# Kernel tuning notes

Hardware: AMD Instinct MI355X
Metric: run time of the kernel (lower is better)

The kernel has to match this reference:

```python
import jax, jax.numpy as jnp
import numpy as np

NOISE_STD = 0.05
ALPHA = 0.2

B, T, I, H, O, R = 64, 1024, 8, 512, 2, 2


def setup_inputs() -> dict:
    key = jax.random.key(0)
    ks = jax.random.split(key, 6)
    return {
        "input": jax.random.normal(ks[0], (B, T, I), dtype=jnp.float32),
        "noise": jax.random.normal(ks[1], (B, T, H), dtype=jnp.float32),
        "wi": jax.random.normal(ks[2], (I, H), dtype=jnp.float32),
        "si": jnp.ones((I,), dtype=jnp.float32),
        "m": jax.random.normal(ks[3], (H, R), dtype=jnp.float32),
        "n": jax.random.normal(ks[4], (H, R), dtype=jnp.float32),
        "wo": jax.random.normal(ks[5], (H, O), dtype=jnp.float32) * 4.0,
        "so": jnp.ones((O,), dtype=jnp.float32),
        "h0": jnp.zeros((H,), dtype=jnp.float32),
    }


def reference(input, noise, wi, si, m, n, wo, so, h0):
    batch, seq_len, _ = input.shape
    hidden = m.shape[0]
    wi_full = wi * si[:, None]          # (I, H)
    wo_full = wo * so                   # (H, O)
    # Precompute input projection for all timesteps: (B, T, H)
    inp_proj = jnp.einsum('bti,ih->bth', input, wi_full)
    h_init = jnp.broadcast_to(h0, (batch, hidden))
    r_init = jnp.tanh(h_init)

    def step(carry, xs):
        h, r = carry
        nz, p = xs  # (B, H) each
        rec = (r @ n) @ m.T / hidden    # rank-r recurrent drive
        h = h + NOISE_STD * nz + ALPHA * (-h + rec + p)
        r = jnp.tanh(h)
        out = r @ wo_full / hidden      # (B, O)
        return (h, r), (out, h)

    xs = (jnp.swapaxes(noise, 0, 1), jnp.swapaxes(inp_proj, 0, 1))  # time-major
    _, (output, traj) = jax.lax.scan(step, (h_init, r_init), xs)
    return jnp.swapaxes(output, 0, 1), jnp.swapaxes(traj, 0, 1)
```

## Files before the change

kernel.cpp:

```cpp
#include <hip/hip_runtime.h>
#include <cstddef>

constexpr int B = 64, T = 1024, I = 8, H = 512, O = 2;
constexpr float ALPHA = 0.2f;
constexpr float NOISE_STD = 0.05f;

constexpr int PF = 8;

template <int CTRL>
__device__ __forceinline__ float dpp_add(float x) {
    int y = __builtin_amdgcn_update_dpp(0, __float_as_int(x), CTRL, 0xF, 0xF, true);
    return x + __int_as_float(y);
}

__device__ __forceinline__ float wave_sum_to_lane63(float x) {
    x = dpp_add<0x111>(x);
    x = dpp_add<0x112>(x);
    x = dpp_add<0x114>(x);
    x = dpp_add<0x118>(x);
    x = dpp_add<0x142>(x);
    x = dpp_add<0x143>(x);
    return x;
}

__device__ __forceinline__ float bcast63(float x) {
    return __int_as_float(__builtin_amdgcn_readlane(__float_as_int(x), 63));
}

__device__ __forceinline__ float fast_tanh(float x) {
    float z = __builtin_amdgcn_exp2f(x * 2.885390081777927f);
    return fmaf(-2.0f, __builtin_amdgcn_rcpf(z + 1.0f), 1.0f);
}

__global__ __launch_bounds__(128)
void precompute_d_kernel(const float* __restrict__ input,
                         const float* __restrict__ noise,
                         const float* __restrict__ wi,
                         const float* __restrict__ si,
                         float* __restrict__ d) {
    const int    bt = blockIdx.x;
    const int    hq = threadIdx.x << 2;

    float x[I];
#pragma unroll
    for (int i = 0; i < I; ++i) x[i] = input[(size_t)bt * I + i] * si[i];

    const size_t off = (size_t)bt * H + hq;
    const float4 nz  = *(const float4*)(noise + off);

    float4 p = make_float4(0.f, 0.f, 0.f, 0.f);
#pragma unroll
    for (int i = 0; i < I; ++i) {
        const float4 w = *(const float4*)(wi + i * H + hq);
        p.x = fmaf(x[i], w.x, p.x);
        p.y = fmaf(x[i], w.y, p.y);
        p.z = fmaf(x[i], w.z, p.z);
        p.w = fmaf(x[i], w.w, p.w);
    }
    float4 o;
    o.x = fmaf(NOISE_STD, nz.x, ALPHA * p.x);
    o.y = fmaf(NOISE_STD, nz.y, ALPHA * p.y);
    o.z = fmaf(NOISE_STD, nz.z, ALPHA * p.z);
    o.w = fmaf(NOISE_STD, nz.w, ALPHA * p.w);
    *(float4*)(d + off) = o;
}

template <bool FUSED>
__global__ __launch_bounds__(64)
void rnn_kernel(const float* __restrict__ dbuf,
                const float* __restrict__ input,
                const float* __restrict__ wi,
                const float* __restrict__ si,
                const float* __restrict__ m,
                const float* __restrict__ n,
                const float* __restrict__ wo,
                const float* __restrict__ so,
                const float* __restrict__ h0,
                float* __restrict__ out,
                float* __restrict__ traj)
{
    const int b    = blockIdx.x;
    const int lane = threadIdx.x;

    constexpr float RS  = ALPHA / (float)H;
    constexpr float OMA = 1.0f - ALPHA;

    const float so0 = so[0] / (float)H;
    const float so1 = so[1] / (float)H;

    float m0s[8], m1s[8], n0[8], n1[8], wo0s[8], wo1s[8], h[8], r[8];
    float wif[I][8];

#pragma unroll
    for (int k = 0; k < 2; ++k) {
#pragma unroll
        for (int c = 0; c < 4; ++c) {
            const int s = k * 4 + c;
            const int j = 256 * k + 4 * lane + c;
            m0s[s]  = m[2 * j + 0] * RS;
            m1s[s]  = m[2 * j + 1] * RS;
            n0[s]   = n[2 * j + 0];
            n1[s]   = n[2 * j + 1];
            wo0s[s] = wo[2 * j + 0] * so0;
            wo1s[s] = wo[2 * j + 1] * so1;
            h[s]    = h0[j];
            r[s]    = tanhf(h[s]);
            if (FUSED) {
#pragma unroll
                for (int i = 0; i < I; ++i) wif[i][s] = wi[i * H + j] * si[i];
            }
        }
    }

    const float* pd    = dbuf + (size_t)b * T * H + 4 * lane;
    float*       ptraj = traj + (size_t)b * T * H + 4 * lane;
    const float* pin   = input + (size_t)b * T * I;
    float*       pout  = out + (size_t)b * T * O;

    float4 buf0[PF], buf1[PF];
#pragma unroll
    for (int u = 0; u < PF; ++u) {
        buf0[u] = *(const float4*)(pd + (size_t)u * H);
        buf1[u] = *(const float4*)(pd + (size_t)u * H + 256);
    }

    static_assert(T % PF == 0, "T must be a multiple of PF");

    for (int tb = 0; tb < T; tb += PF) {
#pragma unroll
        for (int u = 0; u < PF; ++u) {
            const int t = tb + u;

            const float4 cur0 = buf0[u];
            const float4 cur1 = buf1[u];
            if (t + PF < T) {
                buf0[u] = *(const float4*)(pd + (size_t)(t + PF) * H);
                buf1[u] = *(const float4*)(pd + (size_t)(t + PF) * H + 256);
            }

            float pa0a = 0.f, pa1a = 0.f, po0a = 0.f, po1a = 0.f;
            float pa0b = 0.f, pa1b = 0.f, po0b = 0.f, po1b = 0.f;
#pragma unroll
            for (int s = 0; s < 4; ++s) {
                pa0a = fmaf(r[s], n0[s], pa0a);
                pa1a = fmaf(r[s], n1[s], pa1a);
                po0a = fmaf(r[s], wo0s[s], po0a);
                po1a = fmaf(r[s], wo1s[s], po1a);
                pa0b = fmaf(r[s + 4], n0[s + 4], pa0b);
                pa1b = fmaf(r[s + 4], n1[s + 4], pa1b);
                po0b = fmaf(r[s + 4], wo0s[s + 4], po0b);
                po1b = fmaf(r[s + 4], wo1s[s + 4], po1b);
            }
            float ra0 = wave_sum_to_lane63(pa0a + pa0b);
            float ra1 = wave_sum_to_lane63(pa1a + pa1b);
            float ro0 = wave_sum_to_lane63(po0a + po0b);
            float ro1 = wave_sum_to_lane63(po1a + po1b);

            float dv[8];
            if (!FUSED) {
                dv[0] = cur0.x; dv[1] = cur0.y; dv[2] = cur0.z; dv[3] = cur0.w;
                dv[4] = cur1.x; dv[5] = cur1.y; dv[6] = cur1.z; dv[7] = cur1.w;
            } else {
                float x[I];
#pragma unroll
                for (int i = 0; i < I; ++i) x[i] = pin[(size_t)t * I + i];
                const float nzv[8] = {cur0.x, cur0.y, cur0.z, cur0.w,
                                      cur1.x, cur1.y, cur1.z, cur1.w};
#pragma unroll
                for (int s = 0; s < 8; ++s) {
                    float p = 0.f;
#pragma unroll
                    for (int i = 0; i < I; ++i) p = fmaf(x[i], wif[i][s], p);
                    dv[s] = fmaf(NOISE_STD, nzv[s], ALPHA * p);
                }
            }
            float pre[8];
#pragma unroll
            for (int s = 0; s < 8; ++s) pre[s] = fmaf(h[s], OMA, dv[s]);

            if (lane == 63 && t > 0) {
                *(float2*)(pout + (size_t)(t - 1) * O) = make_float2(ro0, ro1);
            }

            const float a0 = bcast63(ra0);
            const float a1 = bcast63(ra1);

#pragma unroll
            for (int s = 0; s < 8; ++s) {
                h[s] = fmaf(a1, m1s[s], fmaf(a0, m0s[s], pre[s]));
                r[s] = fast_tanh(h[s]);
            }

            *(float4*)(ptraj + (size_t)t * H + 0)   = make_float4(h[0], h[1], h[2], h[3]);
            *(float4*)(ptraj + (size_t)t * H + 256) = make_float4(h[4], h[5], h[6], h[7]);
        }
    }

    float po0 = 0.f, po1 = 0.f;
#pragma unroll
    for (int s = 0; s < 8; ++s) {
        po0 = fmaf(r[s], wo0s[s], po0);
        po1 = fmaf(r[s], wo1s[s], po1);
    }
    po0 = wave_sum_to_lane63(po0);
    po1 = wave_sum_to_lane63(po1);
    if (lane == 63) {
        *(float2*)(pout + (size_t)(T - 1) * O) = make_float2(po0, po1);
    }
}

extern "C" void kernel_launch(void* const* d_in, const int* in_sizes, int n_in,
                              void* d_out, int out_size, void* d_ws, size_t ws_size,
                              hipStream_t stream) {
    const float* input = (const float*)d_in[0];
    const float* noise = (const float*)d_in[1];
    const float* wi    = (const float*)d_in[2];
    const float* si    = (const float*)d_in[3];
    const float* m     = (const float*)d_in[4];
    const float* n     = (const float*)d_in[5];
    const float* wo    = (const float*)d_in[6];
    const float* so    = (const float*)d_in[7];
    const float* h0    = (const float*)d_in[8];

    float* out  = (float*)d_out;
    float* traj = (float*)d_out + (size_t)B * T * O;

    const size_t d_bytes = (size_t)B * T * H * sizeof(float);

    if (ws_size >= d_bytes) {
        float* dbuf = (float*)d_ws;
        precompute_d_kernel<<<B * T, 128, 0, stream>>>(input, noise, wi, si, dbuf);
        rnn_kernel<false><<<B, 64, 0, stream>>>(dbuf, nullptr, nullptr, nullptr,
                                                m, n, wo, so, h0, out, traj);
    } else {
        rnn_kernel<true><<<B, 64, 0, stream>>>(noise, input, wi, si,
                                               m, n, wo, so, h0, out, traj);
    }
}
```

Measured before the change: 608.2 us.

## Split recurrence across four waves per batch and move output projection to separate kernel

The sequential recurrence kernel now uses 256 threads (four waves) per batch row, so each lane owns 2 hidden units instead of 8. The rank-2 partial sums are combined through double-buffered shared memory with one __syncthreads per step. The output projection (tanh of traj times wo) is removed from the serial loop and computed afterwards by a fully parallel kernel that rereads traj. This shortens the per-step critical path, at the cost of a block barrier each step and an extra pass over the trajectory. The fallback fused kernel is also restructured into a simple one-step prefetch loop.

```diff
diff --git a/kernel.cpp b/kernel.cpp
--- a/kernel.cpp
+++ b/kernel.cpp
@@ -65,19 +65,125 @@
     *(float4*)(d + off) = o;
 }
 
-template <bool FUSED>
-__global__ __launch_bounds__(64)
-void rnn_kernel(const float* __restrict__ dbuf,
-                const float* __restrict__ input,
-                const float* __restrict__ wi,
-                const float* __restrict__ si,
-                const float* __restrict__ m,
-                const float* __restrict__ n,
+__global__ __launch_bounds__(256)
+void rnn4_kernel(const float* __restrict__ dbuf,
+                 const float* __restrict__ m,
+                 const float* __restrict__ n,
+                 const float* __restrict__ h0,
+                 float* __restrict__ traj)
+{
+    const int b    = blockIdx.x;
+    const int w    = threadIdx.x >> 6;
+    const int lane = threadIdx.x & 63;
+    const int j0   = w * 128 + 2 * lane;
+
+    constexpr float RS  = ALPHA / (float)H;
+    constexpr float OMA = 1.0f - ALPHA;
+
+    const float4 mv = *(const float4*)(m + 2 * j0);
+    const float4 nv = *(const float4*)(n + 2 * j0);
+    const float mm0[2] = {mv.x * RS, mv.z * RS};
+    const float mm1[2] = {mv.y * RS, mv.w * RS};
+    const float nn0[2] = {nv.x, nv.z};
+    const float nn1[2] = {nv.y, nv.w};
+
+    const float2 h0v = *(const float2*)(h0 + j0);
+    float h[2] = {h0v.x, h0v.y};
+    float r[2] = {tanhf(h[0]), tanhf(h[1])};
+
+    __shared__ float2 part[2][4];
+
+    const float* pd = dbuf + (size_t)b * T * H + j0;
+    float*       pt = traj + (size_t)b * T * H + j0;
+
+    float2 ring[PF];
+#pragma unroll
+    for (int u = 0; u < PF; ++u) ring[u] = *(const float2*)(pd + (size_t)u * H);
+
+    static_assert(T % PF == 0, "T must be a multiple of PF");
+
+    for (int tb = 0; tb < T; tb += PF) {
+#pragma unroll
+        for (int u = 0; u < PF; ++u) {
+            const int t = tb + u;
+
+            const float2 d = ring[u];
+            if (t + PF < T) ring[u] = *(const float2*)(pd + (size_t)(t + PF) * H);
+
+            float pa0 = fmaf(r[1], nn0[1], r[0] * nn0[0]);
+            float pa1 = fmaf(r[1], nn1[1], r[0] * nn1[0]);
+            pa0 = wave_sum_to_lane63(pa0);
+            pa1 = wave_sum_to_lane63(pa1);
+            if (lane == 63) part[t & 1][w] = make_float2(pa0, pa1);
+
+            const float pre0 = fmaf(h[0], OMA, d.x);
+            const float pre1 = fmaf(h[1], OMA, d.y);
+
+            __syncthreads();
+
+            const float4 q0 = *(const float4*)&part[t & 1][0];
+            const float4 q1 = *(const float4*)&part[t & 1][2];
+            const float a0 = (q0.x + q0.z) + (q1.x + q1.z);
+            const float a1 = (q0.y + q0.w) + (q1.y + q1.w);
+
+            h[0] = fmaf(a1, mm1[0], fmaf(a0, mm0[0], pre0));
+            h[1] = fmaf(a1, mm1[1], fmaf(a0, mm0[1], pre1));
+            r[0] = fast_tanh(h[0]);
+            r[1] = fast_tanh(h[1]);
+
+            *(float2*)(pt + (size_t)t * H) = make_float2(h[0], h[1]);
+        }
+    }
+}
+
+__global__ __launch_bounds__(256)
+void out_kernel(const float* __restrict__ traj,
                 const float* __restrict__ wo,
                 const float* __restrict__ so,
-                const float* __restrict__ h0,
-                float* __restrict__ out,
-                float* __restrict__ traj)
+                float* __restrict__ out) {
+    const int bt   = blockIdx.x * 4 + (threadIdx.x >> 6);
+    const int lane = threadIdx.x & 63;
+
+    const float so0 = so[0] / (float)H;
+    const float so1 = so[1] / (float)H;
+
+    const float* pt = traj + (size_t)bt * H;
+
+    float o0 = 0.f, o1 = 0.f;
+#pragma unroll
+    for (int k = 0; k < 2; ++k) {
+        const int j = 256 * k + 4 * lane;
+        const float4 hv = *(const float4*)(pt + j);
+        const float4 w0 = *(const float4*)(wo + 2 * j);
+        const float4 w1 = *(const float4*)(wo + 2 * j + 4);
+        const float r0 = fast_tanh(hv.x);
+        const float r1 = fast_tanh(hv.y);
+        const float r2 = fast_tanh(hv.z);
+        const float r3 = fast_tanh(hv.w);
+        o0 = fmaf(r0, w0.x, o0); o1 = fmaf(r0, w0.y, o1);
+        o0 = fmaf(r1, w0.z, o0); o1 = fmaf(r1, w0.w, o1);
+        o0 = fmaf(r2, w1.x, o0); o1 = fmaf(r2, w1.y, o1);
+        o0 = fmaf(r3, w1.z, o0); o1 = fmaf(r3, w1.w, o1);
+    }
+    o0 = wave_sum_to_lane63(o0);
+    o1 = wave_sum_to_lane63(o1);
+    if (lane == 63) {
+        *(float2*)(out + (size_t)bt * O) = make_float2(o0 * so0, o1 * so1);
+    }
+}
+
+__global__ __launch_bounds__(64)
+void rnn_fused_kernel(const float* __restrict__ noise,
+                      const float* __restrict__ input,
+                      const float* __restrict__ wi,
+                      const float* __restrict__ si,
+                      const float* __restrict__ m,
+                      const float* __restrict__ n,
+                      const float* __restrict__ wo,
+                      const float* __restrict__ so,
+                      const float* __restrict__ h0,
+                      float* __restrict__ out,
+                      float* __restrict__ traj)
 {
     const int b    = blockIdx.x;
     const int lane = threadIdx.x;
@@ -105,95 +211,78 @@
             wo1s[s] = wo[2 * j + 1] * so1;
             h[s]    = h0[j];
             r[s]    = tanhf(h[s]);
-            if (FUSED) {
-#pragma unroll
-                for (int i = 0; i < I; ++i) wif[i][s] = wi[i * H + j] * si[i];
-            }
-        }
-    }
-
-    const float* pd    = dbuf + (size_t)b * T * H + 4 * lane;
+#pragma unroll
+            for (int i = 0; i < I; ++i) wif[i][s] = wi[i * H + j] * si[i];
+        }
+    }
+
+    const float* pn    = noise + (size_t)b * T * H + 4 * lane;
     float*       ptraj = traj + (size_t)b * T * H + 4 * lane;
     const float* pin   = input + (size_t)b * T * I;
     float*       pout  = out + (size_t)b * T * O;
 
-    float4 buf0[PF], buf1[PF];
-#pragma unroll
-    for (int u = 0; u < PF; ++u) {
-        buf0[u] = *(const float4*)(pd + (size_t)u * H);
-        buf1[u] = *(const float4*)(pd + (size_t)u * H + 256);
-    }
-
-    static_assert(T % PF == 0, "T must be a multiple of PF");
-
-    for (int tb = 0; tb < T; tb += PF) {
-#pragma unroll
-        for (int u = 0; u < PF; ++u) {
-            const int t = tb + u;
-
-            const float4 cur0 = buf0[u];
-            const float4 cur1 = buf1[u];
-            if (t + PF < T) {
-                buf0[u] = *(const float4*)(pd + (size_t)(t + PF) * H);
-                buf1[u] = *(const float4*)(pd + (size_t)(t + PF) * H + 256);
-            }
-
-            float pa0a = 0.f, pa1a = 0.f, po0a = 0.f, po1a = 0.f;
-            float pa0b = 0.f, pa1b = 0.f, po0b = 0.f, po1b = 0.f;
-#pragma unroll
-            for (int s = 0; s < 4; ++s) {
-                pa0a = fmaf(r[s], n0[s], pa0a);
-                pa1a = fmaf(r[s], n1[s], pa1a);
-                po0a = fmaf(r[s], wo0s[s], po0a);
-                po1a = fmaf(r[s], wo1s[s], po1a);
-                pa0b = fmaf(r[s + 4], n0[s + 4], pa0b);
-                pa1b = fmaf(r[s + 4], n1[s + 4], pa1b);
-                po0b = fmaf(r[s + 4], wo0s[s + 4], po0b);
-                po1b = fmaf(r[s + 4], wo1s[s + 4], po1b);
-            }
-            float ra0 = wave_sum_to_lane63(pa0a + pa0b);
-            float ra1 = wave_sum_to_lane63(pa1a + pa1b);
-            float ro0 = wave_sum_to_lane63(po0a + po0b);
-            float ro1 = wave_sum_to_lane63(po1a + po1b);
-
-            float dv[8];
-            if (!FUSED) {
-                dv[0] = cur0.x; dv[1] = cur0.y; dv[2] = cur0.z; dv[3] = cur0.w;
-                dv[4] = cur1.x; dv[5] = cur1.y; dv[6] = cur1.z; dv[7] = cur1.w;
-            } else {
-                float x[I];
-#pragma unroll
-                for (int i = 0; i < I; ++i) x[i] = pin[(size_t)t * I + i];
-                const float nzv[8] = {cur0.x, cur0.y, cur0.z, cur0.w,
-                                      cur1.x, cur1.y, cur1.z, cur1.w};
-#pragma unroll
-                for (int s = 0; s < 8; ++s) {
-                    float p = 0.f;
-#pragma unroll
-                    for (int i = 0; i < I; ++i) p = fmaf(x[i], wif[i][s], p);
-                    dv[s] = fmaf(NOISE_STD, nzv[s], ALPHA * p);
-                }
-            }
-            float pre[8];
-#pragma unroll
-            for (int s = 0; s < 8; ++s) pre[s] = fmaf(h[s], OMA, dv[s]);
-
-            if (lane == 63 && t > 0) {
-                *(float2*)(pout + (size_t)(t - 1) * O) = make_float2(ro0, ro1);
-            }
-
-            const float a0 = bcast63(ra0);
-            const float a1 = bcast63(ra1);
-
-#pragma unroll
-            for (int s = 0; s < 8; ++s) {
-                h[s] = fmaf(a1, m1s[s], fmaf(a0, m0s[s], pre[s]));
-                r[s] = fast_tanh(h[s]);
-            }
-
-            *(float4*)(ptraj + (size_t)t * H + 0)   = make_float4(h[0], h[1], h[2], h[3]);
-            *(float4*)(ptraj + (size_t)t * H + 256) = make_float4(h[4], h[5], h[6], h[7]);
-        }
+    float4 cur0 = *(const float4*)(pn + 0);
+    float4 cur1 = *(const float4*)(pn + 256);
+
+    for (int t = 0; t < T; ++t) {
+        float4 nxt0, nxt1;
+        if (t + 1 < T) {
+            nxt0 = *(const float4*)(pn + (size_t)(t + 1) * H);
+            nxt1 = *(const float4*)(pn + (size_t)(t + 1) * H + 256);
+        }
+
+        float pa0a = 0.f, pa1a = 0.f, po0a = 0.f, po1a = 0.f;
+        float pa0b = 0.f, pa1b = 0.f, po0b = 0.f, po1b = 0.f;
+#pragma unroll
+        for (int s = 0; s < 4; ++s) {
+            pa0a = fmaf(r[s], n0[s], pa0a);
+            pa1a = fmaf(r[s], n1[s], pa1a);
+            po0a = fmaf(r[s], wo0s[s], po0a);
+            po1a = fmaf(r[s], wo1s[s], po1a);
+            pa0b = fmaf(r[s + 4], n0[s + 4], pa0b);
+            pa1b = fmaf(r[s + 4], n1[s + 4], pa1b);
+            po0b = fmaf(r[s + 4], wo0s[s + 4], po0b);
+            po1b = fmaf(r[s + 4], wo1s[s + 4], po1b);
+        }
+        float ra0 = wave_sum_to_lane63(pa0a + pa0b);
+        float ra1 = wave_sum_to_lane63(pa1a + pa1b);
+        float ro0 = wave_sum_to_lane63(po0a + po0b);
+        float ro1 = wave_sum_to_lane63(po1a + po1b);
+
+        if (lane == 63 && t > 0) {
+            *(float2*)(pout + (size_t)(t - 1) * O) = make_float2(ro0, ro1);
+        }
+
+        const float a0 = bcast63(ra0);
+        const float a1 = bcast63(ra1);
+
+        float x[I];
+#pragma unroll
+        for (int i = 0; i < I; ++i) x[i] = pin[(size_t)t * I + i];
+        const float nzv[8] = {cur0.x, cur0.y, cur0.z, cur0.w,
+                              cur1.x, cur1.y, cur1.z, cur1.w};
+        float dv[8];
+#pragma unroll
+        for (int s = 0; s < 8; ++s) {
+            float p = 0.f;
+#pragma unroll
+            for (int i = 0; i < I; ++i) p = fmaf(x[i], wif[i][s], p);
+            dv[s] = fmaf(NOISE_STD, nzv[s], ALPHA * p);
+        }
+
+#pragma unroll
+        for (int s = 0; s < 8; ++s) {
+            float tmp = fmaf(a0, m0s[s], dv[s]);
+            tmp       = fmaf(a1, m1s[s], tmp);
+            h[s]      = fmaf(h[s], OMA, tmp);
+            r[s]      = fast_tanh(h[s]);
+        }
+
+        *(float4*)(ptraj + (size_t)t * H + 0)   = make_float4(h[0], h[1], h[2], h[3]);
+        *(float4*)(ptraj + (size_t)t * H + 256) = make_float4(h[4], h[5], h[6], h[7]);
+
+        cur0 = nxt0;
+        cur1 = nxt1;
     }
 
     float po0 = 0.f, po1 = 0.f;
@@ -230,10 +319,10 @@
     if (ws_size >= d_bytes) {
         float* dbuf = (float*)d_ws;
         precompute_d_kernel<<<B * T, 128, 0, stream>>>(input, noise, wi, si, dbuf);
-        rnn_kernel<false><<<B, 64, 0, stream>>>(dbuf, nullptr, nullptr, nullptr,
-                                                m, n, wo, so, h0, out, traj);
+        rnn4_kernel<<<B, 256, 0, stream>>>(dbuf, m, n, h0, traj);
+        out_kernel<<<(B * T) / 4, 256, 0, stream>>>(traj, wo, so, out);
     } else {
-        rnn_kernel<true><<<B, 64, 0, stream>>>(noise, input, wi, si,
+        rnn_fused_kernel<<<B, 64, 0, stream>>>(noise, input, wi, si,
                                                m, n, wo, so, h0, out, traj);
     }
 }
```

After: 587.3 us. 3.4% less time.

## Fuse input projection into RNN and split hidden state across four waves per batch

Applied to the files above, without the earlier changes.

Removes the separate precompute kernel and its round trip through a large workspace buffer. The scan kernel now runs 256 threads per batch row, with each lane owning two hidden units, and computes the input projection on the fly from inputs staged in LDS. Each timestep reduces across the four waves through a double-buffered LDS array guarded by a workgroup barrier. This shortens the serial dependency chain and the per-lane work, at the cost of one block barrier per timestep.

```diff
diff --git a/kernel.cpp b/kernel.cpp
--- a/kernel.cpp
+++ b/kernel.cpp
@@ -23,106 +23,74 @@
     return x;
 }
 
-__device__ __forceinline__ float bcast63(float x) {
-    return __int_as_float(__builtin_amdgcn_readlane(__float_as_int(x), 63));
-}
-
 __device__ __forceinline__ float fast_tanh(float x) {
     float z = __builtin_amdgcn_exp2f(x * 2.885390081777927f);
     return fmaf(-2.0f, __builtin_amdgcn_rcpf(z + 1.0f), 1.0f);
 }
 
-__global__ __launch_bounds__(128)
-void precompute_d_kernel(const float* __restrict__ input,
-                         const float* __restrict__ noise,
-                         const float* __restrict__ wi,
-                         const float* __restrict__ si,
-                         float* __restrict__ d) {
-    const int    bt = blockIdx.x;
-    const int    hq = threadIdx.x << 2;
-
-    float x[I];
-#pragma unroll
-    for (int i = 0; i < I; ++i) x[i] = input[(size_t)bt * I + i] * si[i];
-
-    const size_t off = (size_t)bt * H + hq;
-    const float4 nz  = *(const float4*)(noise + off);
-
-    float4 p = make_float4(0.f, 0.f, 0.f, 0.f);
-#pragma unroll
-    for (int i = 0; i < I; ++i) {
-        const float4 w = *(const float4*)(wi + i * H + hq);
-        p.x = fmaf(x[i], w.x, p.x);
-        p.y = fmaf(x[i], w.y, p.y);
-        p.z = fmaf(x[i], w.z, p.z);
-        p.w = fmaf(x[i], w.w, p.w);
-    }
-    float4 o;
-    o.x = fmaf(NOISE_STD, nz.x, ALPHA * p.x);
-    o.y = fmaf(NOISE_STD, nz.y, ALPHA * p.y);
-    o.z = fmaf(NOISE_STD, nz.z, ALPHA * p.z);
-    o.w = fmaf(NOISE_STD, nz.w, ALPHA * p.w);
-    *(float4*)(d + off) = o;
-}
-
-template <bool FUSED>
-__global__ __launch_bounds__(64)
-void rnn_kernel(const float* __restrict__ dbuf,
-                const float* __restrict__ input,
-                const float* __restrict__ wi,
-                const float* __restrict__ si,
-                const float* __restrict__ m,
-                const float* __restrict__ n,
-                const float* __restrict__ wo,
-                const float* __restrict__ so,
-                const float* __restrict__ h0,
-                float* __restrict__ out,
-                float* __restrict__ traj)
+__global__ __launch_bounds__(256)
+void rnn_fused4_kernel(const float* __restrict__ input,
+                       const float* __restrict__ noise,
+                       const float* __restrict__ wi,
+                       const float* __restrict__ si,
+                       const float* __restrict__ m,
+                       const float* __restrict__ n,
+                       const float* __restrict__ wo,
+                       const float* __restrict__ so,
+                       const float* __restrict__ h0,
+                       float* __restrict__ out,
+                       float* __restrict__ traj)
 {
     const int b    = blockIdx.x;
-    const int lane = threadIdx.x;
+    const int w    = threadIdx.x >> 6;
+    const int lane = threadIdx.x & 63;
+    const int j0   = w * 128 + 2 * lane;
+
+    __shared__ float  xin[T * I];
+    __shared__ float4 part[2][4];
+
+    {
+        const float4* src = (const float4*)(input + (size_t)b * T * I);
+        float4*       dst = (float4*)xin;
+#pragma unroll
+        for (int i = 0; i < (T * I / 4) / 256; ++i)
+            dst[threadIdx.x + 256 * i] = src[threadIdx.x + 256 * i];
+    }
+    __syncthreads();
 
     constexpr float RS  = ALPHA / (float)H;
     constexpr float OMA = 1.0f - ALPHA;
-
     const float so0 = so[0] / (float)H;
     const float so1 = so[1] / (float)H;
 
-    float m0s[8], m1s[8], n0[8], n1[8], wo0s[8], wo1s[8], h[8], r[8];
-    float wif[I][8];
-
-#pragma unroll
-    for (int k = 0; k < 2; ++k) {
-#pragma unroll
-        for (int c = 0; c < 4; ++c) {
-            const int s = k * 4 + c;
-            const int j = 256 * k + 4 * lane + c;
-            m0s[s]  = m[2 * j + 0] * RS;
-            m1s[s]  = m[2 * j + 1] * RS;
-            n0[s]   = n[2 * j + 0];
-            n1[s]   = n[2 * j + 1];
-            wo0s[s] = wo[2 * j + 0] * so0;
-            wo1s[s] = wo[2 * j + 1] * so1;
-            h[s]    = h0[j];
-            r[s]    = tanhf(h[s]);
-            if (FUSED) {
-#pragma unroll
-                for (int i = 0; i < I; ++i) wif[i][s] = wi[i * H + j] * si[i];
-            }
-        }
-    }
-
-    const float* pd    = dbuf + (size_t)b * T * H + 4 * lane;
-    float*       ptraj = traj + (size_t)b * T * H + 4 * lane;
-    const float* pin   = input + (size_t)b * T * I;
-    float*       pout  = out + (size_t)b * T * O;
-
-    float4 buf0[PF], buf1[PF];
-#pragma unroll
-    for (int u = 0; u < PF; ++u) {
-        buf0[u] = *(const float4*)(pd + (size_t)u * H);
-        buf1[u] = *(const float4*)(pd + (size_t)u * H + 256);
-    }
+    const float4 mv = *(const float4*)(m + 2 * j0);
+    const float4 nv = *(const float4*)(n + 2 * j0);
+    const float4 wv = *(const float4*)(wo + 2 * j0);
+    const float mm0[2] = {mv.x * RS, mv.z * RS};
+    const float mm1[2] = {mv.y * RS, mv.w * RS};
+    const float nn0[2] = {nv.x, nv.z};
+    const float nn1[2] = {nv.y, nv.w};
+    const float ww0[2] = {wv.x, wv.z};
+    const float ww1[2] = {wv.y, wv.w};
+
+    float wif[I][2];
+#pragma unroll
+    for (int i = 0; i < I; ++i) {
+        wif[i][0] = wi[i * H + j0]     * si[i];
+        wif[i][1] = wi[i * H + j0 + 1] * si[i];
+    }
+
+    const float2 h0v = *(const float2*)(h0 + j0);
+    float h[2] = {h0v.x, h0v.y};
+    float r[2] = {tanhf(h[0]), tanhf(h[1])};
+
+    const float* pn   = noise + (size_t)b * T * H + j0;
+    float*       pt   = traj  + (size_t)b * T * H + j0;
+    float*       pout = out   + (size_t)b * T * O;
+
+    float2 ring[PF];
+#pragma unroll
+    for (int u = 0; u < PF; ++u) ring[u] = *(const float2*)(pn + (size_t)u * H);
 
     static_assert(T % PF == 0, "T must be a multiple of PF");
 
@@ -131,81 +99,84 @@
         for (int u = 0; u < PF; ++u) {
             const int t = tb + u;
 
-            const float4 cur0 = buf0[u];
-            const float4 cur1 = buf1[u];
-            if (t + PF < T) {
-                buf0[u] = *(const float4*)(pd + (size_t)(t + PF) * H);
-                buf1[u] = *(const float4*)(pd + (size_t)(t + PF) * H + 256);
+            const float4 xa = *(const float4*)(xin + t * I);
+            const float4 xb = *(const float4*)(xin + t * I + 4);
+
+            float pa0 = fmaf(r[1], nn0[1], r[0] * nn0[0]);
+            float pa1 = fmaf(r[1], nn1[1], r[0] * nn1[0]);
+            float po0 = fmaf(r[1], ww0[1], r[0] * ww0[0]);
+            float po1 = fmaf(r[1], ww1[1], r[0] * ww1[0]);
+
+            const float2 nz = ring[u];
+            if (t + PF < T) ring[u] = *(const float2*)(pn + (size_t)(t + PF) * H);
+
+            pa0 = wave_sum_to_lane63(pa0);
+            pa1 = wave_sum_to_lane63(pa1);
+            po0 = wave_sum_to_lane63(po0);
+            po1 = wave_sum_to_lane63(po1);
+
+            const float x0 = xa.x, x1 = xa.y, x2 = xa.z, x3 = xa.w;
+            const float x4 = xb.x, x5 = xb.y, x6 = xb.z, x7 = xb.w;
+            float acc0 = x0 * wif[0][0], acc1 = x0 * wif[0][1];
+            acc0 = fmaf(x1, wif[1][0], acc0); acc1 = fmaf(x1, wif[1][1], acc1);
+            acc0 = fmaf(x2, wif[2][0], acc0); acc1 = fmaf(x2, wif[2][1], acc1);
+            acc0 = fmaf(x3, wif[3][0], acc0); acc1 = fmaf(x3, wif[3][1], acc1);
+            acc0 = fmaf(x4, wif[4][0], acc0); acc1 = fmaf(x4, wif[4][1], acc1);
+            acc0 = fmaf(x5, wif[5][0], acc0); acc1 = fmaf(x5, wif[5][1], acc1);
+            acc0 = fmaf(x6, wif[6][0], acc0); acc1 = fmaf(x6, wif[6][1], acc1);
+            acc0 = fmaf(x7, wif[7][0], acc0); acc1 = fmaf(x7, wif[7][1], acc1);
+            const float dv0 = fmaf(NOISE_STD, nz.x, ALPHA * acc0);
+            const float dv1 = fmaf(NOISE_STD, nz.y, ALPHA * acc1);
+            const float pre0 = fmaf(h[0], OMA, dv0);
+            const float pre1 = fmaf(h[1], OMA, dv1);
+
+            if (lane == 63) part[t & 1][w] = make_float4(pa0, pa1, po0, po1);
+
+            __builtin_amdgcn_sched_barrier(0);
+            asm volatile("s_waitcnt lgkmcnt(0)" ::: "memory");
+            __builtin_amdgcn_s_barrier();
+            __builtin_amdgcn_sched_barrier(0);
+
+            const float4 q0 = part[t & 1][0];
+            const float4 q1 = part[t & 1][1];
+            const float4 q2 = part[t & 1][2];
+            const float4 q3 = part[t & 1][3];
+            const float a0 = (q0.x + q1.x) + (q2.x + q3.x);
+            const float a1 = (q0.y + q1.y) + (q2.y + q3.y);
+
+            if (t > 0 && threadIdx.x == 63) {
+                const float o0 = (q0.z + q1.z) + (q2.z + q3.z);
+                const float o1 = (q0.w + q1.w) + (q2.w + q3.w);
+                *(float2*)(pout + (size_t)(t - 1) * O) =
+                    make_float2(o0 * so0, o1 * so1);
             }
 
-            float pa0a = 0.f, pa1a = 0.f, po0a = 0.f, po1a = 0.f;
-            float pa0b = 0.f, pa1b = 0.f, po0b = 0.f, po1b = 0.f;
-#pragma unroll
-            for (int s = 0; s < 4; ++s) {
-                pa0a = fmaf(r[s], n0[s], pa0a);
-                pa1a = fmaf(r[s], n1[s], pa1a);
-                po0a = fmaf(r[s], wo0s[s], po0a);
-                po1a = fmaf(r[s], wo1s[s], po1a);
-                pa0b = fmaf(r[s + 4], n0[s + 4], pa0b);
-                pa1b = fmaf(r[s + 4], n1[s + 4], pa1b);
-                po0b = fmaf(r[s + 4], wo0s[s + 4], po0b);
-                po1b = fmaf(r[s + 4], wo1s[s + 4], po1b);
-            }
-            float ra0 = wave_sum_to_lane63(pa0a + pa0b);
-            float ra1 = wave_sum_to_lane63(pa1a + pa1b);
-            float ro0 = wave_sum_to_lane63(po0a + po0b);
-            float ro1 = wave_sum_to_lane63(po1a + po1b);
-
-            float dv[8];
-            if (!FUSED) {
-                dv[0] = cur0.x; dv[1] = cur0.y; dv[2] = cur0.z; dv[3] = cur0.w;
-                dv[4] = cur1.x; dv[5] = cur1.y; dv[6] = cur1.z; dv[7] = cur1.w;
-            } else {
-                float x[I];
-#pragma unroll
-                for (int i = 0; i < I; ++i) x[i] = pin[(size_t)t * I + i];
-                const float nzv[8] = {cur0.x, cur0.y, cur0.z, cur0.w,
-                                      cur1.x, cur1.y, cur1.z, cur1.w};
-#pragma unroll
-                for (int s = 0; s < 8; ++s) {
-                    float p = 0.f;
-#pragma unroll
-                    for (int i = 0; i < I; ++i) p = fmaf(x[i], wif[i][s], p);
-                    dv[s] = fmaf(NOISE_STD, nzv[s], ALPHA * p);
-                }
-            }
-            float pre[8];
-#pragma unroll
-            for (int s = 0; s < 8; ++s) pre[s] = fmaf(h[s], OMA, dv[s]);
-
-            if (lane == 63 && t > 0) {
-                *(float2*)(pout + (size_t)(t - 1) * O) = make_float2(ro0, ro1);
-            }
-
-            const float a0 = bcast63(ra0);
-            const float a1 = bcast63(ra1);
-
-#pragma unroll
-            for (int s = 0; s < 8; ++s) {
-                h[s] = fmaf(a1, m1s[s], fmaf(a0, m0s[s], pre[s]));
-                r[s] = fast_tanh(h[s]);
-            }
-
-            *(float4*)(ptraj + (size_t)t * H + 0)   = make_float4(h[0], h[1], h[2], h[3]);
-            *(float4*)(ptraj + (size_t)t * H + 256) = make_float4(h[4], h[5], h[6], h[7]);
+            h[0] = fmaf(a1, mm1[0], fmaf(a0, mm0[0], pre0));
+            h[1] = fmaf(a1, mm1[1], fmaf(a0, mm0[1], pre1));
+            r[0] = fast_tanh(h[0]);
+            r[1] = fast_tanh(h[1]);
+
+            *(float2*)(pt + (size_t)t * H) = make_float2(h[0], h[1]);
         }
     }
 
-    float po0 = 0.f, po1 = 0.f;
-#pragma unroll
-    for (int s = 0; s < 8; ++s) {
-        po0 = fmaf(r[s], wo0s[s], po0);
-        po1 = fmaf(r[s], wo1s[s], po1);
-    }
-    po0 = wave_sum_to_lane63(po0);
-    po1 = wave_sum_to_lane63(po1);
-    if (lane == 63) {
-        *(float2*)(pout + (size_t)(T - 1) * O) = make_float2(po0, po1);
+    {
+        float po0 = fmaf(r[1], ww0[1], r[0] * ww0[0]);
+        float po1 = fmaf(r[1], ww1[1], r[0] * ww1[0]);
+        po0 = wave_sum_to_lane63(po0);
+        po1 = wave_sum_to_lane63(po1);
+        if (lane == 63) part[0][w] = make_float4(po0, po1, 0.f, 0.f);
+        __syncthreads();
+        if (threadIdx.x == 0) {
+            const float4 q0 = part[0][0];
+            const float4 q1 = part[0][1];
+            const float4 q2 = part[0][2];
+            const float4 q3 = part[0][3];
+            const float o0 = (q0.x + q1.x) + (q2.x + q3.x);
+            const float o1 = (q0.y + q1.y) + (q2.y + q3.y);
+            *(float2*)(pout + (size_t)(T - 1) * O) =
+                make_float2(o0 * so0, o1 * so1);
+        }
     }
 }
 
@@ -225,15 +196,8 @@
     float* out  = (float*)d_out;
     float* traj = (float*)d_out + (size_t)B * T * O;
 
-    const size_t d_bytes = (size_t)B * T * H * sizeof(float);
-
-    if (ws_size >= d_bytes) {
-        float* dbuf = (float*)d_ws;
-        precompute_d_kernel<<<B * T, 128, 0, stream>>>(input, noise, wi, si, dbuf);
-        rnn_kernel<false><<<B, 64, 0, stream>>>(dbuf, nullptr, nullptr, nullptr,
-                                                m, n, wo, so, h0, out, traj);
-    } else {
-        rnn_kernel<true><<<B, 64, 0, stream>>>(noise, input, wi, si,
-                                               m, n, wo, so, h0, out, traj);
-    }
-}
+    (void)d_ws; (void)ws_size;
+
+    rnn_fused4_kernel<<<B, 256, 0, stream>>>(input, noise, wi, si,
+                                             m, n, wo, so, h0, out, traj);
+}
```

Result: faster. 560.9 us (-7.8%).
